# Kernel tuning notes

Measured on AMD Instinct MI355X. Metric: run time of the kernel, lower is better.

Reference implementation:

```python
import jax, jax.numpy as jnp
import numpy as np

CHUNK = 128
EPS = 1e-6


def setup_inputs() -> dict:
    key = jax.random.key(0)
    k1, k2, k3 = jax.random.split(key, 3)
    B, H, N, D, E = 4, 8, 4096, 64, 64
    q = jax.random.uniform(k1, (B, H, N, D), dtype=jnp.float32)
    k = jax.random.uniform(k2, (B, H, N, D), dtype=jnp.float32)
    v = jax.random.normal(k3, (B, H, N, E), dtype=jnp.float32)
    return {"q": q, "k": k, "v": v, "inferrring_states": 1}


def reference(q, k, v, inferrring_states):
    # infer_hidden_states path: chunked causal linear attention with carried state.
    B, H, N, D = q.shape
    E = v.shape[-1]
    nc = N // CHUNK
    # [nc, B, H, CHUNK, *] for scan over chunks
    qc = jnp.moveaxis(q.reshape(B, H, nc, CHUNK, D), 2, 0)
    kc = jnp.moveaxis(k.reshape(B, H, nc, CHUNK, D), 2, 0)
    vc = jnp.moveaxis(v.reshape(B, H, nc, CHUNK, E), 2, 0)

    Z0 = jnp.zeros((B, H, 1, D), dtype=q.dtype)        # running sum of k
    S0 = jnp.zeros((B, H, 1, D, E), dtype=q.dtype)     # running sum of k v^T

    def step(carry, qkv):
        Z, S = carry
        qi, ki, vi = qkv
        k_cumsum = Z + jnp.cumsum(ki, axis=-2)                      # [B,H,C,D]
        D_inv = 1.0 / jnp.einsum('bhnd,bhnd->bhn', qi, k_cumsum + EPS)
        context = jnp.einsum('bhnd,bhne->bhnde', ki, vi)            # [B,H,C,D,E]
        ctx_cumsum = S + jnp.cumsum(context, axis=-3)
        out = jnp.einsum('bhnde,bhnd,bhn->bhne', ctx_cumsum, qi, D_inv)
        new_carry = (k_cumsum[:, :, -1:], ctx_cumsum[:, :, -1:])
        return new_carry, out

    (Z, S), outs = jax.lax.scan(step, (Z0, S0), (qc, kc, vc))
    out = jnp.moveaxis(outs, 0, 2).reshape(B, H, N, E)
    # states: Z=[B,H,D], S=[B,H,D,E]
    return out, Z[:, :, 0], S[:, :, 0]
```

## Files before the change

kernel.cpp:

```cpp
#include <hip/hip_runtime.h>


#define CHUNKSZ 128
#define DD 64
#define EE 64
#define NC 32
#define NBH 32
#define NSEQ 4096
#define EPSV 1e-6f
#define OUT0 (NBH * NSEQ * EE)
#define KV_ELEMS (NBH * NC * DD * EE)

typedef short bf16x8 __attribute__((ext_vector_type(8)));
typedef short bf16x4 __attribute__((ext_vector_type(4)));
typedef float f32x4  __attribute__((ext_vector_type(4)));

__device__ __forceinline__ unsigned short f2bf(float f) {
    union { float f; unsigned u; } x; x.f = f;
    unsigned u = x.u + 0x7FFFu + ((x.u >> 16) & 1u);
    return (unsigned short)(u >> 16);
}
__device__ __forceinline__ float bf2f(unsigned short s) {
    union { unsigned u; float f; } x; x.u = ((unsigned)s) << 16;
    return x.f;
}

__global__ __launch_bounds__(256) void la_phase1(
    const float* __restrict__ k, const float* __restrict__ v,
    unsigned short* __restrict__ kvT, float* __restrict__ ks)
{
    const int blk = blockIdx.x;
    const int bh = blk / NC, c = blk % NC;
    const size_t rowbase = (size_t)bh * NSEQ + (size_t)c * CHUNKSZ;

    __shared__ alignas(16) unsigned short kT[CHUNKSZ * DD];
    __shared__ alignas(16) unsigned short vT[CHUNKSZ * EE];
    __shared__ float ksp[4][DD];

    char* kb = (char*)kT;
    char* vb = (char*)vT;

    const int t = threadIdx.x;
    const int w = t >> 6, l = t & 63;
    const int lg = l >> 4, lm = l & 15;
    const int col = t & 63;

    float kpart = 0.f;
#pragma unroll
    for (int pass = 0; pass < 4; ++pass) {
        const int mg = w + 4 * pass;
        const float* kp = k + (rowbase + mg * 8) * DD + col;
        const float* vp = v + (rowbase + mg * 8) * EE + col;
        float kf[8], vf[8];
#pragma unroll
        for (int j = 0; j < 8; ++j) kf[j] = kp[(size_t)j * DD];
#pragma unroll
        for (int j = 0; j < 8; ++j) vf[j] = vp[(size_t)j * EE];
        bf16x8 ku, vu;
#pragma unroll
        for (int j = 0; j < 8; ++j) {
            kpart += kf[j];
            ku[j] = (short)f2bf(kf[j]);
            vu[j] = (short)f2bf(vf[j]);
        }
        *(bf16x8*)(kb + mg * 1024 + col * 16) = ku;
        *(bf16x8*)(vb + mg * 1024 + col * 16) = vu;
    }
    ksp[w][col] = kpart;
    __syncthreads();

    f32x4 acc[4] = {};
#pragma unroll
    for (int kk = 0; kk < 4; ++kk) {
        bf16x8 aK = *(bf16x8*)(kb + (lg + 4 * kk) * 1024 + (16 * w + lm) * 16);
#pragma unroll
        for (int ei = 0; ei < 4; ++ei) {
            bf16x8 bV = *(bf16x8*)(vb + (lg + 4 * kk) * 1024 + (16 * ei + lm) * 16);
            acc[ei] = __builtin_amdgcn_mfma_f32_16x16x32_bf16(aK, bV, acc[ei], 0, 0, 0);
        }
    }
    unsigned short* kvout = kvT + (size_t)(bh * NC + c) * DD * EE;
#pragma unroll
    for (int ei = 0; ei < 4; ++ei) {
        bf16x4 u;
        u[0] = (short)f2bf(acc[ei][0]); u[1] = (short)f2bf(acc[ei][1]);
        u[2] = (short)f2bf(acc[ei][2]); u[3] = (short)f2bf(acc[ei][3]);
        *(bf16x4*)(kvout + (16 * ei + lm) * DD + 16 * w + 4 * lg) = u;
    }
    if (t < DD)
        ks[(size_t)(bh * NC + c) * DD + t] = ksp[0][t] + ksp[1][t] + ksp[2][t] + ksp[3][t];
}

__global__ __launch_bounds__(64) void la_phase2(
    unsigned short* __restrict__ kvT, float* __restrict__ ks, float* __restrict__ out)
{
    const int bid = blockIdx.x, t = threadIdx.x;
    if (bid < 256) {
        const int gid = bid * 64 + t;
        const int bh = gid >> 9;
        const int g = gid & 511;
        unsigned short* base = kvT + (size_t)bh * (NC * DD * EE) + (size_t)g * 8;
        bf16x8 vals[NC];
#pragma unroll
        for (int c = 0; c < NC; ++c)
            vals[c] = *(const bf16x8*)(base + (size_t)c * (DD * EE));
        float run[8] = {};
#pragma unroll
        for (int c = 0; c < NC; ++c) {
            bf16x8 pr;
#pragma unroll
            for (int j = 0; j < 8; ++j) pr[j] = (short)f2bf(run[j]);
            *(bf16x8*)(base + (size_t)c * (DD * EE)) = pr;
#pragma unroll
            for (int j = 0; j < 8; ++j) run[j] += bf2f((unsigned short)vals[c][j]);
        }
        const int e = g >> 3, d0 = (g & 7) * 8;
        float* Sout = out + OUT0 + NBH * DD + (size_t)bh * DD * EE;
#pragma unroll
        for (int j = 0; j < 8; ++j)
            Sout[(size_t)(d0 + j) * EE + e] = run[j];
    } else {
        const int tid = (bid - 256) * 64 + t;
        const int bh = tid >> 6, d = tid & 63;
        float vals[NC];
#pragma unroll
        for (int c = 0; c < NC; ++c)
            vals[c] = ks[(size_t)(bh * NC + c) * DD + d];
        float run = 0.f;
#pragma unroll
        for (int c = 0; c < NC; ++c) {
            float x = vals[c];
            ks[(size_t)(bh * NC + c) * DD + d] = run;
            run += x;
        }
        out[OUT0 + tid] = run;
    }
}

__global__ __launch_bounds__(256) void la_phase3(
    const float* __restrict__ q, const float* __restrict__ k,
    const float* __restrict__ v, const unsigned short* __restrict__ kvT,
    const float* __restrict__ ks, float* __restrict__ out)
{
    const int blk = blockIdx.x;
    const int bh = blk / NC, c = blk % NC;
    const size_t rowbase = (size_t)bh * NSEQ + (size_t)c * CHUNKSZ;

    __shared__ alignas(16) unsigned short k_lds[CHUNKSZ * DD];
    __shared__ alignas(16) unsigned short v_lds[CHUNKSZ * EE];
    __shared__ alignas(16) unsigned short s_lds[CHUNKSZ * CHUNKSZ];
    __shared__ alignas(16) unsigned short st_lds[DD * EE];
    __shared__ float dinv_lds[CHUNKSZ];
    __shared__ float zi_lds[DD];

    char* kb  = (char*)k_lds;
    char* vb  = (char*)v_lds;
    char* sb  = (char*)s_lds;
    char* stb = (char*)st_lds;

    const int t  = threadIdx.x;
    const int w  = t >> 6;
    const int l  = t & 63;
    const int lg = l >> 4;
    const int lm = l & 15;

    {
        bf16x8 z = {0,0,0,0,0,0,0,0};
#pragma unroll
        for (int i = 0; i < 8; ++i)
            *(bf16x8*)(sb + t * 128 + i * 16) = z;
    }
    {
        const float4* kg = (const float4*)(k + rowbase * DD);
#pragma unroll
        for (int i = 0; i < 8; ++i) {
            int idx = t + i * 256;
            int m = idx >> 4, c4 = idx & 15;
            float4 f = kg[idx];
            bf16x4 u;
            u[0] = (short)f2bf(f.x); u[1] = (short)f2bf(f.y);
            u[2] = (short)f2bf(f.z); u[3] = (short)f2bf(f.w);
            int byt = m * 128 + ((c4 * 8) ^ ((m & 7) << 4));
            *(bf16x4*)(kb + byt) = u;
        }
    }
    {
        const int col = t & 63;
#pragma unroll
        for (int pass = 0; pass < 4; ++pass) {
            const int mg = (t >> 6) + 4 * pass;
            const float* vp = v + (rowbase + mg * 8) * EE + col;
            float vf[8];
#pragma unroll
            for (int j = 0; j < 8; ++j) vf[j] = vp[(size_t)j * EE];
            bf16x8 u;
#pragma unroll
            for (int j = 0; j < 8; ++j) u[j] = (short)f2bf(vf[j]);
            *(bf16x8*)(vb + mg * 1024 + col * 16) = u;
        }
    }
    {
        const unsigned short* sg = kvT + (size_t)(bh * NC + c) * DD * EE;
#pragma unroll
        for (int i = 0; i < 2; ++i) {
            int idx = t + 256 * i;
            int e = idx >> 3;
            bf16x8 x = *(const bf16x8*)(sg + (size_t)idx * 8);
            int byt = e * 128 + (((idx & 7) * 16) ^ ((e & 7) << 4));
            *(bf16x8*)(stb + byt) = x;
        }
    }
    if (t < DD) zi_lds[t] = ks[(size_t)(bh * NC + c) * DD + t];

    bf16x8 a_q[2][2];
#pragma unroll
    for (int ni2 = 0; ni2 < 2; ++ni2) {
        int ni = w + 4 * ni2;
        const float* qrow = q + (rowbase + 16 * ni + lm) * DD;
#pragma unroll
        for (int kk = 0; kk < 2; ++kk) {
            const float4* p = (const float4*)(qrow + 8 * lg + 32 * kk);
            float4 f0 = p[0], f1 = p[1];
            bf16x8 u;
            u[0] = (short)f2bf(f0.x); u[1] = (short)f2bf(f0.y);
            u[2] = (short)f2bf(f0.z); u[3] = (short)f2bf(f0.w);
            u[4] = (short)f2bf(f1.x); u[5] = (short)f2bf(f1.y);
            u[6] = (short)f2bf(f1.z); u[7] = (short)f2bf(f1.w);
            a_q[ni2][kk] = u;
        }
    }
    __syncthreads();

#pragma unroll
    for (int ni2 = 0; ni2 < 2; ++ni2) {
        const int ni = w + 4 * ni2;
        const int n = 16 * ni + lm;
        float rsum = 0.f;
        for (int mi = 0; mi <= ni; ++mi) {
            f32x4 cc = {0.f, 0.f, 0.f, 0.f};
            const int mrow = 16 * mi + lm;
#pragma unroll
            for (int kk = 0; kk < 2; ++kk) {
                int byt = mrow * 128 + (((8 * lg + 32 * kk) * 2) ^ ((mrow & 7) << 4));
                bf16x8 ak = *(bf16x8*)(kb + byt);
                cc = __builtin_amdgcn_mfma_f32_16x16x32_bf16(ak, a_q[ni2][kk], cc, 0, 0, 0);
            }
            const int m0 = 16 * mi + 4 * lg;
            bf16x4 u;
#pragma unroll
            for (int r = 0; r < 4; ++r) {
                float val = (m0 + r <= n) ? cc[r] : 0.f;
                u[r] = (short)f2bf(val);
                rsum += val;
            }
            *(bf16x4*)(sb + n * 256 + ((m0 * 2) ^ ((n & 7) << 4))) = u;
        }
        float qz = 0.f, qs = 0.f;
#pragma unroll
        for (int kk = 0; kk < 2; ++kk) {
#pragma unroll
            for (int i = 0; i < 8; ++i) {
                float qf = bf2f((unsigned short)a_q[ni2][kk][i]);
                qz += qf * zi_lds[8 * lg + 32 * kk + i];
                qs += qf;
            }
        }
        float part = rsum + qz + EPSV * qs;
        part += __shfl_xor(part, 16);
        part += __shfl_xor(part, 32);
        if (lg == 0) dinv_lds[n] = 1.f / part;
    }
    __syncthreads();

    f32x4 acc[2][4];
#pragma unroll
    for (int ni2 = 0; ni2 < 2; ++ni2) {
        const int ni = w + 4 * ni2;
        const int kmax = (ni >> 1) + 1;
#pragma unroll
        for (int ei = 0; ei < 4; ++ei) {
            f32x4 cc = {0.f, 0.f, 0.f, 0.f};
            const int e = 16 * ei + lm;
#pragma unroll
            for (int kk = 0; kk < 2; ++kk) {
                int byt = e * 128 + (((8 * lg + 32 * kk) * 2) ^ ((e & 7) << 4));
                bf16x8 bs = *(bf16x8*)(stb + byt);
                cc = __builtin_amdgcn_mfma_f32_16x16x32_bf16(a_q[ni2][kk], bs, cc, 0, 0, 0);
            }
            const int n = 16 * ni + lm;
            for (int kk = 0; kk < kmax; ++kk) {
                int bytA = n * 256 + (((8 * lg + 32 * kk) * 2) ^ ((n & 7) << 4));
                bf16x8 as = *(bf16x8*)(sb + bytA);
                int bytB = (lg + 4 * kk) * 1024 + e * 16;
                bf16x8 bv = *(bf16x8*)(vb + bytB);
                cc = __builtin_amdgcn_mfma_f32_16x16x32_bf16(as, bv, cc, 0, 0, 0);
            }
            acc[ni2][ei] = cc;
        }
    }
    __syncthreads();

#pragma unroll
    for (int ni2 = 0; ni2 < 2; ++ni2) {
        const int nbase = 16 * (w + 4 * ni2) + 4 * lg;
#pragma unroll
        for (int ei = 0; ei < 4; ++ei) {
            const int e = 16 * ei + lm;
#pragma unroll
            for (int r = 0; r < 4; ++r) {
                int n = nbase + r;
                out[(rowbase + n) * EE + e] = acc[ni2][ei][r] * dinv_lds[n];
            }
        }
    }
}

extern "C" void kernel_launch(void* const* d_in, const int* in_sizes, int n_in,
                              void* d_out, int out_size, void* d_ws, size_t ws_size,
                              hipStream_t stream)
{
    (void)in_sizes; (void)n_in; (void)out_size; (void)ws_size;
    const float* q = (const float*)d_in[0];
    const float* k = (const float*)d_in[1];
    const float* v = (const float*)d_in[2];
    float* out = (float*)d_out;
    unsigned short* kvT = (unsigned short*)d_ws;
    float* ks = (float*)(kvT + KV_ELEMS);

    la_phase1<<<NBH * NC, 256, 0, stream>>>(k, v, kvT, ks);
    la_phase2<<<288, 64, 0, stream>>>(kvT, ks, out);
    la_phase3<<<NBH * NC, 256, 0, stream>>>(q, k, v, kvT, ks, out);
}
```

Before: 50.60 us.

## Fold chunk-state prefix scan into phase3 and drop the phase2 kernel

Removes the separate prefix-scan kernel. Each phase3 block now sums all preceding chunk kv tiles and k-sums itself, keeping the result in registers as the MFMA B operand, and the last chunk writes the final states. This also adds an XCD-aware block index remap (phys&7) in phase1 and phase3. The goal is to save one kernel launch and the round trip through global memory, at the cost of redundant quadratic reads of kv tiles: later chunks read up to 31 tiles each.

```diff
diff --git a/kernel.cpp b/kernel.cpp
--- a/kernel.cpp
+++ b/kernel.cpp
@@ -29,8 +29,9 @@
     const float* __restrict__ k, const float* __restrict__ v,
     unsigned short* __restrict__ kvT, float* __restrict__ ks)
 {
-    const int blk = blockIdx.x;
-    const int bh = blk / NC, c = blk % NC;
+    const int phys = blockIdx.x;
+    const int blk  = (phys & 7) * 128 + (phys >> 3);
+    const int bh = blk >> 5, c = blk & 31;
     const size_t rowbase = (size_t)bh * NSEQ + (size_t)c * CHUNKSZ;
 
     __shared__ alignas(16) unsigned short kT[CHUNKSZ * DD];
@@ -91,78 +92,92 @@
         ks[(size_t)(bh * NC + c) * DD + t] = ksp[0][t] + ksp[1][t] + ksp[2][t] + ksp[3][t];
 }
 
-__global__ __launch_bounds__(64) void la_phase2(
-    unsigned short* __restrict__ kvT, float* __restrict__ ks, float* __restrict__ out)
-{
-    const int bid = blockIdx.x, t = threadIdx.x;
-    if (bid < 256) {
-        const int gid = bid * 64 + t;
-        const int bh = gid >> 9;
-        const int g = gid & 511;
-        unsigned short* base = kvT + (size_t)bh * (NC * DD * EE) + (size_t)g * 8;
-        bf16x8 vals[NC];
-#pragma unroll
-        for (int c = 0; c < NC; ++c)
-            vals[c] = *(const bf16x8*)(base + (size_t)c * (DD * EE));
-        float run[8] = {};
-#pragma unroll
-        for (int c = 0; c < NC; ++c) {
-            bf16x8 pr;
-#pragma unroll
-            for (int j = 0; j < 8; ++j) pr[j] = (short)f2bf(run[j]);
-            *(bf16x8*)(base + (size_t)c * (DD * EE)) = pr;
-#pragma unroll
-            for (int j = 0; j < 8; ++j) run[j] += bf2f((unsigned short)vals[c][j]);
-        }
-        const int e = g >> 3, d0 = (g & 7) * 8;
-        float* Sout = out + OUT0 + NBH * DD + (size_t)bh * DD * EE;
-#pragma unroll
-        for (int j = 0; j < 8; ++j)
-            Sout[(size_t)(d0 + j) * EE + e] = run[j];
-    } else {
-        const int tid = (bid - 256) * 64 + t;
-        const int bh = tid >> 6, d = tid & 63;
-        float vals[NC];
-#pragma unroll
-        for (int c = 0; c < NC; ++c)
-            vals[c] = ks[(size_t)(bh * NC + c) * DD + d];
-        float run = 0.f;
-#pragma unroll
-        for (int c = 0; c < NC; ++c) {
-            float x = vals[c];
-            ks[(size_t)(bh * NC + c) * DD + d] = run;
-            run += x;
-        }
-        out[OUT0 + tid] = run;
-    }
-}
-
 __global__ __launch_bounds__(256) void la_phase3(
     const float* __restrict__ q, const float* __restrict__ k,
     const float* __restrict__ v, const unsigned short* __restrict__ kvT,
     const float* __restrict__ ks, float* __restrict__ out)
 {
-    const int blk = blockIdx.x;
-    const int bh = blk / NC, c = blk % NC;
+    const int phys = blockIdx.x;
+    const int blk  = (phys & 7) * 128 + (phys >> 3);
+    const int bh = blk >> 5, c = blk & 31;
     const size_t rowbase = (size_t)bh * NSEQ + (size_t)c * CHUNKSZ;
 
     __shared__ alignas(16) unsigned short k_lds[CHUNKSZ * DD];
     __shared__ alignas(16) unsigned short v_lds[CHUNKSZ * EE];
     __shared__ alignas(16) unsigned short s_lds[CHUNKSZ * CHUNKSZ];
-    __shared__ alignas(16) unsigned short st_lds[DD * EE];
     __shared__ float dinv_lds[CHUNKSZ];
     __shared__ float zi_lds[DD];
 
     char* kb  = (char*)k_lds;
     char* vb  = (char*)v_lds;
     char* sb  = (char*)s_lds;
-    char* stb = (char*)st_lds;
 
     const int t  = threadIdx.x;
     const int w  = t >> 6;
     const int l  = t & 63;
     const int lg = l >> 4;
     const int lm = l & 15;
+
+    float stf[4][2][8];
+#pragma unroll
+    for (int ei = 0; ei < 4; ++ei)
+#pragma unroll
+        for (int kk = 0; kk < 2; ++kk)
+#pragma unroll
+            for (int i = 0; i < 8; ++i) stf[ei][kk][i] = 0.f;
+    {
+        const unsigned short* tiles = kvT + (size_t)bh * NC * DD * EE;
+        const int eoff0 = (16 * 0 + lm) * 64 + 8 * lg;
+        for (int j = 0; j < c; ++j) {
+            const unsigned short* tj = tiles + (size_t)j * DD * EE;
+#pragma unroll
+            for (int ei = 0; ei < 4; ++ei) {
+#pragma unroll
+                for (int kk = 0; kk < 2; ++kk) {
+                    bf16x8 x = *(const bf16x8*)(tj + eoff0 + ei * 1024 + kk * 32);
+#pragma unroll
+                    for (int i = 0; i < 8; ++i)
+                        stf[ei][kk][i] += bf2f((unsigned short)x[i]);
+                }
+            }
+        }
+    }
+    if (t < DD) {
+        const float* kp = ks + (size_t)bh * NC * DD + t;
+        float z = 0.f;
+        for (int j = 0; j < c; ++j) z += kp[(size_t)j * DD];
+        zi_lds[t] = z;
+        if (c == NC - 1)
+            out[OUT0 + (size_t)bh * DD + t] = z + kp[(size_t)(NC - 1) * DD];
+    }
+    if (c == NC - 1) {
+        const unsigned short* t31 = kvT + ((size_t)bh * NC + NC - 1) * DD * EE;
+        float* Sout = out + OUT0 + NBH * DD + (size_t)bh * DD * EE;
+        const int eoff0 = lm * 64 + 8 * lg;
+#pragma unroll
+        for (int ei = 0; ei < 4; ++ei) {
+#pragma unroll
+            for (int kk = 0; kk < 2; ++kk) {
+                bf16x8 x = *(const bf16x8*)(t31 + eoff0 + ei * 1024 + kk * 32);
+                const int e = 16 * ei + lm;
+#pragma unroll
+                for (int i = 0; i < 8; ++i) {
+                    int d = 8 * lg + 32 * kk + i;
+                    Sout[(size_t)d * EE + e] = stf[ei][kk][i] + bf2f((unsigned short)x[i]);
+                }
+            }
+        }
+    }
+    bf16x8 b_st[4][2];
+#pragma unroll
+    for (int ei = 0; ei < 4; ++ei)
+#pragma unroll
+        for (int kk = 0; kk < 2; ++kk) {
+            bf16x8 u;
+#pragma unroll
+            for (int i = 0; i < 8; ++i) u[i] = (short)f2bf(stf[ei][kk][i]);
+            b_st[ei][kk] = u;
+        }
 
     {
         bf16x8 z = {0,0,0,0,0,0,0,0};
@@ -199,19 +214,6 @@
             *(bf16x8*)(vb + mg * 1024 + col * 16) = u;
         }
     }
-    {
-        const unsigned short* sg = kvT + (size_t)(bh * NC + c) * DD * EE;
-#pragma unroll
-        for (int i = 0; i < 2; ++i) {
-            int idx = t + 256 * i;
-            int e = idx >> 3;
-            bf16x8 x = *(const bf16x8*)(sg + (size_t)idx * 8);
-            int byt = e * 128 + (((idx & 7) * 16) ^ ((e & 7) << 4));
-            *(bf16x8*)(stb + byt) = x;
-        }
-    }
-    if (t < DD) zi_lds[t] = ks[(size_t)(bh * NC + c) * DD + t];
-
     bf16x8 a_q[2][2];
 #pragma unroll
     for (int ni2 = 0; ni2 < 2; ++ni2) {
@@ -282,11 +284,8 @@
             f32x4 cc = {0.f, 0.f, 0.f, 0.f};
             const int e = 16 * ei + lm;
 #pragma unroll
-            for (int kk = 0; kk < 2; ++kk) {
-                int byt = e * 128 + (((8 * lg + 32 * kk) * 2) ^ ((e & 7) << 4));
-                bf16x8 bs = *(bf16x8*)(stb + byt);
-                cc = __builtin_amdgcn_mfma_f32_16x16x32_bf16(a_q[ni2][kk], bs, cc, 0, 0, 0);
-            }
+            for (int kk = 0; kk < 2; ++kk)
+                cc = __builtin_amdgcn_mfma_f32_16x16x32_bf16(a_q[ni2][kk], b_st[ei][kk], cc, 0, 0, 0);
             const int n = 16 * ni + lm;
             for (int kk = 0; kk < kmax; ++kk) {
                 int bytA = n * 256 + (((8 * lg + 32 * kk) * 2) ^ ((n & 7) << 4));
@@ -328,6 +327,5 @@
     float* ks = (float*)(kvT + KV_ELEMS);
 
     la_phase1<<<NBH * NC, 256, 0, stream>>>(k, v, kvT, ks);
-    la_phase2<<<288, 64, 0, stream>>>(kvT, ks, out);
     la_phase3<<<NBH * NC, 256, 0, stream>>>(q, k, v, kvT, ks, out);
 }
```

After: 130.1 us. 157% more time.
